# Performance work log

Hardware: AMD Instinct MI355X
Metric: run time of the kernel (lower is better)

## Reference

```python
import jax, jax.numpy as jnp
import numpy as np

B, T, C = 2, 1024, 2048
HEAD = 64              # args.head_size_a
H = C // HEAD          # n_head = 32
D_DECAY, D_AAA, D_MV, D_GATE = 96, 96, 64, 256
GN_EPS = 0.00064
EPS_NORM = 1e-12

ARGS = ['x', 'v0', 'xx_r', 'xx_w', 'xx_k', 'xx_v', 'xx_a', 'xx_g',
        'ww_b', 'ww_w1', 'ww_w2', 'aa_b', 'aa_w1', 'aa_w2',
        'vv_b', 'vv_w1', 'vv_w2', 'gg_w1', 'gg_w2',
        'kk_s', 'ka_s', 'rk_s', 'W_r', 'W_k', 'W_v', 'W_o', 'gn_w', 'gn_b']


def setup_inputs() -> dict:
    key = jax.random.key(0)
    it = iter(jax.random.split(key, 32))
    nrm = lambda shape, s=1.0: jax.random.normal(next(it), shape, jnp.float32) * s
    d = {'x': nrm((B, T, C)), 'v0': nrm((B, T, C))}
    for nm in ('xx_r', 'xx_w', 'xx_k', 'xx_v', 'xx_a', 'xx_g',
               'ww_b', 'aa_b', 'vv_b', 'kk_s', 'ka_s'):
        d[nm] = nrm((1, 1, C), 0.5)
    d['ww_w1'] = nrm((C, D_DECAY), 0.02); d['ww_w2'] = nrm((D_DECAY, C), 0.02)
    d['aa_w1'] = nrm((C, D_AAA), 0.02);   d['aa_w2'] = nrm((D_AAA, C), 0.02)
    d['vv_w1'] = nrm((C, D_MV), 0.02);    d['vv_w2'] = nrm((D_MV, C), 0.02)
    d['gg_w1'] = nrm((C, D_GATE), 0.02);  d['gg_w2'] = nrm((D_GATE, C), 0.02)
    d['rk_s'] = nrm((H, HEAD), 0.5)
    d['W_r'] = nrm((C, C), 0.02); d['W_k'] = nrm((C, C), 0.02)
    d['W_v'] = nrm((C, C), 0.02); d['W_o'] = nrm((C, C), 0.02)
    d['gn_w'] = jnp.ones((C,), jnp.float32)
    d['gn_b'] = jnp.zeros((C,), jnp.float32)
    return d


def _rwkv7_op(r, w, k, v, a, b):
    # RWKV7 state recurrence: state[b,h,i,j] (i = value dim, j = key dim),
    # vectorized over (B,H,N), scanned over T.
    to_tbhn = lambda t: t.reshape(B, T, H, HEAD).astype(jnp.float32).transpose(1, 0, 2, 3)
    rT, kT, vT, aT, bT = map(to_tbhn, (r, k, v, a, b))
    wT = jnp.exp(-jnp.exp(to_tbhn(w)))   # decay in (0, 1)
    state0 = jnp.zeros((B, H, HEAD, HEAD), jnp.float32)

    def step(state, inp):
        wt, kt, vt, at, bt, rt = inp     # each [B,H,N]
        sa = jnp.einsum('bhij,bhj->bhi', state, at)
        state = (state * wt[:, :, None, :]
                 + sa[..., None] * bt[:, :, None, :]
                 + vt[..., None] * kt[:, :, None, :])
        return state, jnp.einsum('bhij,bhj->bhi', state, rt)

    _, outs = jax.lax.scan(step, state0, (wT, kT, vT, aT, bT, rT))  # [T,B,H,N]
    return outs.transpose(1, 0, 2, 3).reshape(B, T, C)


def _group_norm(y, gn_w, gn_b):
    # GroupNorm(H, C, eps=0.00064) applied on (B*T, C): per-(token, head) stats over N
    yh = y.reshape(B, T, H, HEAD)
    mu = yh.mean(-1, keepdims=True)
    var = yh.var(-1, keepdims=True)
    yh = (yh - mu) * jax.lax.rsqrt(var + GN_EPS)
    yh = yh * gn_w.reshape(1, 1, H, HEAD) + gn_b.reshape(1, 1, H, HEAD)
    return yh.reshape(B, T, C)


def _forward(x, v0, xx_r, xx_w, xx_k, xx_v, xx_a, xx_g,
             ww_b, ww_w1, ww_w2, aa_b, aa_w1, aa_w2,
             vv_b, vv_w1, vv_w2, gg_w1, gg_w2,
             kk_s, ka_s, rk_s, W_r, W_k, W_v, W_o, gn_w, gn_b):
    # time_shift(x) - x : shift sequence right by one with zero pad
    xx = jnp.pad(x, ((0, 0), (1, 0), (0, 0)))[:, :T, :] - x
    xr = x + xx * xx_r; xw = x + xx * xx_w; xk = x + xx * xx_k
    xv = x + xx * xx_v; xa = x + xx * xx_a; xg = x + xx * xx_g

    r = xr @ W_r
    w = -jax.nn.softplus(-(ww_b + jnp.tanh(xw @ ww_w1) @ ww_w2)) - 0.5  # clamp to (-inf,-0.5)
    k = xk @ W_k
    v = xv @ W_v
    # layer_id > 0: mix with layer-0 value residual
    v = v + (v0 - v) * jax.nn.sigmoid(vv_b + (xv @ vv_w1) @ vv_w2)
    a = jax.nn.sigmoid(aa_b + (xa @ aa_w1) @ aa_w2)
    g = jax.nn.sigmoid(xg @ gg_w1) @ gg_w2

    kk = k * kk_s
    kkh = kk.reshape(B, T, H, HEAD)
    kk = (kkh / jnp.maximum(jnp.linalg.norm(kkh, axis=-1, keepdims=True), EPS_NORM)).reshape(B, T, C)
    k = k * (1.0 + (a - 1.0) * ka_s)

    y = _rwkv7_op(r, w, k, v, -kk, kk * a)
    y = _group_norm(y, gn_w, gn_b)
    # per-head bonus: (r*k*rk_s).sum(-1) * v
    bonus = ((r.reshape(B, T, H, HEAD) * k.reshape(B, T, H, HEAD) * rk_s).sum(-1, keepdims=True)
             * v.reshape(B, T, H, HEAD)).reshape(B, T, C)
    y = y + bonus
    return (y * g) @ W_o


def reference(x, v0, xx_r, xx_w, xx_k, xx_v, xx_a, xx_g,
              ww_b, ww_w1, ww_w2, aa_b, aa_w1, aa_w2,
              vv_b, vv_w1, vv_w2, gg_w1, gg_w2,
              kk_s, ka_s, rk_s, W_r, W_k, W_v, W_o, gn_w, gn_b):
    out = _forward(x, v0, xx_r, xx_w, xx_k, xx_v, xx_a, xx_g,
                   ww_b, ww_w1, ww_w2, aa_b, aa_w1, aa_w2,
                   vv_b, vv_w1, vv_w2, gg_w1, gg_w2,
                   kk_s, ka_s, rk_s, W_r, W_k, W_v, W_o, gn_w, gn_b)
    # layer_id > 0 passes v0 through unchanged
    return (out, v0)
```

## Files before the change

kernel.cpp:

```cpp
#include <hip/hip_runtime.h>
#include <hip/hip_bf16.h>
#include <math.h>

typedef unsigned short u16;
typedef __attribute__((ext_vector_type(4))) unsigned short us4;
typedef __attribute__((ext_vector_type(8))) unsigned short us8;
typedef __attribute__((ext_vector_type(8))) short s8v;
typedef __attribute__((ext_vector_type(4))) float f4v;

#define BB 2
#define TT 1024
#define CC 2048
#define HH 32
#define BT (BB*TT)


__device__ __forceinline__ float bf2f(u16 u) {
  return __uint_as_float(((unsigned int)u) << 16);
}
__device__ __forceinline__ u16 f2bf(float f) {
  unsigned int x = __float_as_uint(f);
  x += 0x7fffu + ((x >> 16) & 1u);
  return (u16)(x >> 16);
}

__device__ __forceinline__ void gload16(const u16* g, u16* l) {
  __builtin_amdgcn_global_load_lds(
      (const __attribute__((address_space(1))) void*)g,
      (__attribute__((address_space(3))) void*)l, 16, 0, 0);
}

__global__ __launch_bounds__(256)
void mix_k(const float* __restrict__ x, const float* __restrict__ s,
           u16* __restrict__ out) {
  int idx = blockIdx.x * 256 + threadIdx.x;
  int c = idx & (CC - 1);
  int t = (idx >> 11) & (TT - 1);
  float xv = x[idx];
  float xp = (t == 0) ? 0.f : x[idx - CC];
  out[idx] = f2bf(xv + (xp - xv) * s[c]);
}

__global__ __launch_bounds__(256)
void wt_k(const float* __restrict__ W, u16* __restrict__ Wt, int K, int N,
          int Kp) {
  __shared__ u16 tile[32][36];
  const int k0 = blockIdx.x * 32, n0 = blockIdx.y * 32;
  const int tid = threadIdx.x;
  const int r = tid >> 3, c4 = (tid & 7) << 2;
  float4 v = *(const float4*)(W + (size_t)(k0 + r) * N + n0 + c4);
  tile[r][c4 + 0] = f2bf(v.x); tile[r][c4 + 1] = f2bf(v.y);
  tile[r][c4 + 2] = f2bf(v.z); tile[r][c4 + 3] = f2bf(v.w);
  __syncthreads();
  ushort4 o;
  o.x = tile[c4 + 0][r]; o.y = tile[c4 + 1][r];
  o.z = tile[c4 + 2][r]; o.w = tile[c4 + 3][r];
  *(ushort4*)(Wt + (size_t)(n0 + r) * Kp + k0 + c4) = o;
}

enum { EPI_BF = 0, EPI_F32 = 1, EPI_BIAS_SP = 2, EPI_BIAS_SIG = 3,
       EPI_VMIX = 4 };

template<int EPI>
__global__ __launch_bounds__(256)
void mgemm_k(const u16* __restrict__ A, const u16* __restrict__ Bt,
             float* __restrict__ outF, u16* __restrict__ outB,
             int M, int N, int K, int lda, int ldb,
             const float* __restrict__ bias, const u16* __restrict__ p1,
             const float* __restrict__ p2)
{
  __shared__ alignas(16) u16 As[128 * 64];
  __shared__ alignas(16) u16 Bs[128 * 64];
  const int m0 = blockIdx.x * 128;
  const int n0 = blockIdx.y * 128;
  const int tid = threadIdx.x;
  const int lane = tid & 63;
  const int wid = tid >> 6;
  const int wr = wid >> 1, wc = wid & 1;
  f4v acc[4][4];
  #pragma unroll
  for (int i = 0; i < 4; ++i)
    #pragma unroll
    for (int j = 0; j < 4; ++j) acc[i][j] = f4v{0.f, 0.f, 0.f, 0.f};

  const int l15 = lane & 15;
  const int lq = lane >> 4;
  const int nkt = K >> 6;
  for (int kt = 0; kt < nkt; ++kt) {
    const int k0 = kt << 6;
    __syncthreads();
    #pragma unroll
    for (int a = 0; a < 4; ++a) {
      const int blkU = (wid * 4 + a) * 64;
      const int U = blkU + lane;
      const int row = U >> 3;
      const int u = U & 7;
      const int col = ((u ^ (row & 7)) << 3);
      gload16(A  + (size_t)(m0 + row) * lda + k0 + col, &As[blkU * 8]);
      gload16(Bt + (size_t)(n0 + row) * ldb + k0 + col, &Bs[blkU * 8]);
    }
    __syncthreads();
    #pragma unroll
    for (int h = 0; h < 2; ++h) {
      s8v af[4], bfr[4];
      #pragma unroll
      for (int i = 0; i < 4; ++i) {
        const int row = wr * 64 + i * 16 + l15;
        const int u = (h * 4 + lq) ^ (row & 7);
        af[i] = *(const s8v*)&As[row * 64 + u * 8];
      }
      #pragma unroll
      for (int j = 0; j < 4; ++j) {
        const int row = wc * 64 + j * 16 + l15;
        const int u = (h * 4 + lq) ^ (row & 7);
        bfr[j] = *(const s8v*)&Bs[row * 64 + u * 8];
      }
      #pragma unroll
      for (int i = 0; i < 4; ++i)
        #pragma unroll
        for (int j = 0; j < 4; ++j)
          acc[i][j] = __builtin_amdgcn_mfma_f32_16x16x32_bf16(af[i], bfr[j],
                                                              acc[i][j],
                                                              0, 0, 0);
    }
  }
  const int rbase = m0 + wr * 64 + (lq << 2);
  const int cbase = n0 + wc * 64 + l15;
  #pragma unroll
  for (int i = 0; i < 4; ++i) {
    #pragma unroll
    for (int j = 0; j < 4; ++j) {
      f4v c = acc[i][j];
      const int col = cbase + j * 16;
      #pragma unroll
      for (int q = 0; q < 4; ++q) {
        const int row = rbase + i * 16 + q;
        const size_t idx = (size_t)row * N + col;
        const float r = c[q];
        if (EPI == EPI_BF) {
          outB[idx] = f2bf(r);
        } else if (EPI == EPI_F32) {
          outF[idx] = r;
        } else if (EPI == EPI_BIAS_SP) {
          float u = bias[col] + r;
          float z = -u;
          float sp = fmaxf(z, 0.f) + log1pf(expf(-fabsf(z)));
          outB[idx] = f2bf(-sp - 0.5f);
        } else if (EPI == EPI_BIAS_SIG) {
          float u = bias[col] + r;
          outB[idx] = f2bf(1.f / (1.f + expf(-u)));
        } else if (EPI == EPI_VMIX) {
          float u = bias[col] + r;
          float sg = 1.f / (1.f + expf(-u));
          float v = bf2f(p1[idx]);
          float v0v = p2[idx];
          outB[idx] = f2bf(v + (v0v - v) * sg);
        }
      }
    }
  }
}

__global__ __launch_bounds__(256)
void gemm_part_k(const u16* __restrict__ A, const float* __restrict__ W,
                 float* __restrict__ outF, int M, int N, int K, int kchunk,
                 int NP)
{
  __shared__ alignas(16) float As[16][68];
  __shared__ alignas(16) float Bs[16][68];
  const int m0 = blockIdx.x * 64;
  const int n0 = blockIdx.y * 64;
  const int kz = blockIdx.z;
  const int k0base = kz * kchunk;
  const int tid = threadIdx.x;
  const int tx = tid & 15, ty = tid >> 4;
  float acc[4][4] = {{0.f}};
  const int a_m = tid >> 2;
  const int a_k = (tid & 3) << 2;
  const int b_k = tid >> 4;
  const int b_n = (tid & 15) << 2;
  const int niters = kchunk >> 4;
  for (int it = 0; it < niters; ++it) {
    const int k0 = k0base + (it << 4);
    float4 av;
    {
      ushort4 u = *(const ushort4*)(A + (size_t)(m0 + a_m) * K + (k0 + a_k));
      av = make_float4(bf2f(u.x), bf2f(u.y), bf2f(u.z), bf2f(u.w));
    }
    float4 bv;
    {
      int gn = n0 + b_n;
      const float* wp = W + (size_t)(k0 + b_k) * N + gn;
      if (gn + 3 < N) {
        bv = *(const float4*)wp;
      } else {
        bv.x = (gn + 0 < N) ? wp[0] : 0.f;
        bv.y = (gn + 1 < N) ? wp[1] : 0.f;
        bv.z = (gn + 2 < N) ? wp[2] : 0.f;
        bv.w = (gn + 3 < N) ? wp[3] : 0.f;
      }
    }
    __syncthreads();
    As[a_k + 0][a_m] = av.x; As[a_k + 1][a_m] = av.y;
    As[a_k + 2][a_m] = av.z; As[a_k + 3][a_m] = av.w;
    Bs[b_k][b_n + 0] = bv.x; Bs[b_k][b_n + 1] = bv.y;
    Bs[b_k][b_n + 2] = bv.z; Bs[b_k][b_n + 3] = bv.w;
    __syncthreads();
    #pragma unroll
    for (int kk = 0; kk < 16; ++kk) {
      float4 a4 = *(const float4*)&As[kk][ty << 2];
      float4 b4 = *(const float4*)&Bs[kk][tx << 2];
      float ar[4] = {a4.x, a4.y, a4.z, a4.w};
      float br[4] = {b4.x, b4.y, b4.z, b4.w};
      #pragma unroll
      for (int i = 0; i < 4; ++i)
        #pragma unroll
        for (int j = 0; j < 4; ++j)
          acc[i][j] = fmaf(ar[i], br[j], acc[i][j]);
    }
  }
  #pragma unroll
  for (int i = 0; i < 4; ++i) {
    int gm = m0 + (ty << 2) + i;
    #pragma unroll
    for (int j = 0; j < 4; ++j) {
      int gn = n0 + (tx << 2) + j;
      if (gn >= N) continue;
      outF[((size_t)kz * M + gm) * NP + gn] = acc[i][j];
    }
  }
}

__global__ __launch_bounds__(256)
void reduce_k(const float* __restrict__ part, u16* __restrict__ out,
              int M, int D, int NP, int nz, int act, int Dp)
{
  int idx = blockIdx.x * 256 + threadIdx.x;
  if (idx >= M * Dp) return;
  int t = idx / Dp, n = idx - t * Dp;
  float s = 0.f;
  if (n < D) {
    for (int z = 0; z < nz; ++z) s += part[((size_t)z * M + t) * NP + n];
    if (act == 1) s = tanhf(s);
    else if (act == 2) s = 1.f / (1.f + expf(-s));
  }
  out[idx] = f2bf(s);
}

__global__ __launch_bounds__(256)
void prep12_k(const u16* __restrict__ k_in, const u16* __restrict__ a_in,
              const u16* __restrict__ r_in, const u16* __restrict__ w_in,
              const float* __restrict__ kk_s, const float* __restrict__ ka_s,
              u16* __restrict__ ao_out, u16* __restrict__ bo_out,
              u16* __restrict__ k_out, u16* __restrict__ wd_out,
              u16* __restrict__ rw_out, float2* __restrict__ scal,
              float4* __restrict__ scal4)
{
  const int tid = threadIdx.x;
  const int lane = tid & 63;
  const int hpidx = blockIdx.x * 4 + (tid >> 6);
  const int h = hpidx & (HH - 1);
  const int btp = hpidx >> 5;
  const int tp = btp & (TT / 2 - 1);
  const int b = btp >> 9;
  const int c = (h << 6) + lane;
  const size_t be = ((size_t)(b * TT + 2 * tp)) * CC + (h << 6) + lane;
  const size_t bod = be + CC;
  const float ks = kk_s[c], kas = ka_s[c];
  const float k1 = bf2f(k_in[be]),  k2 = bf2f(k_in[bod]);
  const float a1 = bf2f(a_in[be]),  a2 = bf2f(a_in[bod]);
  const float r1 = bf2f(r_in[be]),  r2 = bf2f(r_in[bod]);
  const float wraw1 = bf2f(w_in[be]), wraw2 = bf2f(w_in[bod]);
  float kk1 = k1 * ks, kk2 = k2 * ks;
  float ss1 = kk1 * kk1, ss2 = kk2 * kk2;
  #pragma unroll
  for (int off = 32; off; off >>= 1) {
    ss1 += __shfl_xor(ss1, off, 64);
    ss2 += __shfl_xor(ss2, off, 64);
  }
  const float kkn1 = kk1 / fmaxf(sqrtf(ss1), 1e-12f);
  const float kkn2 = kk2 / fmaxf(sqrtf(ss2), 1e-12f);
  const float kf1 = k1 * (1.f + (a1 - 1.f) * kas);
  const float kf2 = k2 * (1.f + (a2 - 1.f) * kas);
  const float wd1 = expf(-expf(wraw1));
  const float wd2 = expf(-expf(wraw2));
  const float ao1 = -kkn1, ao2 = -kkn2;
  const float bo1 = kkn1 * a1, bo2 = kkn2 * a2;
  const float rw1 = wd1 * r1, rw2 = wd2 * r2;
  float kr1 = kf1 * r1, br1 = bo1 * r1;
  float kr2 = kf2 * r2, br2 = bo2 * r2;
  float cba = bo1 * ao2, ckb = kf1 * ao2;
  float crb = bo1 * rw2, crk = kf1 * rw2;
  #pragma unroll
  for (int off = 32; off; off >>= 1) {
    kr1 += __shfl_xor(kr1, off, 64);  br1 += __shfl_xor(br1, off, 64);
    kr2 += __shfl_xor(kr2, off, 64);  br2 += __shfl_xor(br2, off, 64);
    cba += __shfl_xor(cba, off, 64);  ckb += __shfl_xor(ckb, off, 64);
    crb += __shfl_xor(crb, off, 64);  crk += __shfl_xor(crk, off, 64);
  }
  ao_out[be]  = f2bf(ao1);
  ao_out[bod] = f2bf(wd1 * ao2);
  bo_out[be]  = f2bf(bo1 * wd2);
  bo_out[bod] = f2bf(bo2);
  k_out[be]   = f2bf(kf1);
  k_out[bod]  = f2bf(kf2);
  wd_out[be]  = f2bf(wd1 * wd2);
  wd_out[bod] = f2bf(kf1 * wd2);
  rw_out[be]  = f2bf(rw1);
  rw_out[bod] = f2bf(wd1 * rw2);
  if (lane == 0) {
    const int se = (b * TT + 2 * tp) * HH + h;
    scal[se]      = make_float2(kr1, br1);
    scal[se + HH] = make_float2(kr2, br2);
    scal4[hpidx]  = make_float4(cba, ckb, crb, crk);
  }
}

__global__ __launch_bounds__(256)
void rec_k(const u16* __restrict__ rw, const u16* __restrict__ wd,
           const u16* __restrict__ kv, const u16* __restrict__ v,
           const u16* __restrict__ ao, const u16* __restrict__ bo,
           const float2* __restrict__ scal, const float4* __restrict__ scal4,
           u16* __restrict__ y)
{
  const int gw = blockIdx.x * 4 + (threadIdx.x >> 6);
  const int lane = threadIdx.x & 63;
  const int sub = lane & 15;
  const int grp = lane >> 4;
  const int bh = gw >> 4;
  const int rblk = gw & 15;
  const int i = rblk * 4 + grp;
  const int b = bh >> 5, h = bh & (HH - 1);
  const size_t base0 = ((size_t)b * TT) * CC + (h << 6);
  const size_t vecb = base0 + (sub << 2);
  const size_t vb   = base0 + i;
  const int sbase = b * TT * HH + h;
  const int pbase = b * (TT / 2) * HH + h;
  float s0 = 0.f, s1 = 0.f, s2 = 0.f, s3 = 0.f;

  us4 W12, KW1, AO1, WA2, BW1, BO2, RW1, WR2, K2;
  float V1, V2; float2 SE, SO; float4 S4;
#define PLOAD(TP) do {                                                  \
    const size_t be_ = vecb + (size_t)(2 * (TP)) * CC;                  \
    const size_t bo_ = be_ + CC;                                        \
    W12 = *(const us4*)(wd + be_);  KW1 = *(const us4*)(wd + bo_);      \
    AO1 = *(const us4*)(ao + be_);  WA2 = *(const us4*)(ao + bo_);      \
    BW1 = *(const us4*)(bo + be_);  BO2 = *(const us4*)(bo + bo_);      \
    RW1 = *(const us4*)(rw + be_);  WR2 = *(const us4*)(rw + bo_);      \
    K2  = *(const us4*)(kv + bo_);                                      \
    V1 = bf2f(v[vb + (size_t)(2 * (TP)) * CC]);                         \
    V2 = bf2f(v[vb + (size_t)(2 * (TP) + 1) * CC]);                     \
    SE = scal[sbase + (2 * (TP)) * HH];                                 \
    SO = scal[sbase + (2 * (TP) + 1) * HH];                             \
    S4 = scal4[pbase + (TP) * HH];                                      \
  } while (0)

  PLOAD(0);
  for (int tp = 0; tp < TT / 2; ++tp) {
    const float w0 = bf2f(W12[0]), w1 = bf2f(W12[1]),
                w2 = bf2f(W12[2]), w3 = bf2f(W12[3]);
    const float kw0 = bf2f(KW1[0]), kw1_ = bf2f(KW1[1]),
                kw2 = bf2f(KW1[2]), kw3 = bf2f(KW1[3]);
    const float a0 = bf2f(AO1[0]), a1 = bf2f(AO1[1]),
                a2 = bf2f(AO1[2]), a3 = bf2f(AO1[3]);
    const float x0 = bf2f(WA2[0]), x1 = bf2f(WA2[1]),
                x2 = bf2f(WA2[2]), x3 = bf2f(WA2[3]);
    const float bw0 = bf2f(BW1[0]), bw1_ = bf2f(BW1[1]),
                bw2 = bf2f(BW1[2]), bw3 = bf2f(BW1[3]);
    const float b0 = bf2f(BO2[0]), b1 = bf2f(BO2[1]),
                b2 = bf2f(BO2[2]), b3 = bf2f(BO2[3]);
    const float e0 = bf2f(RW1[0]), e1 = bf2f(RW1[1]),
                e2 = bf2f(RW1[2]), e3 = bf2f(RW1[3]);
    const float f0 = bf2f(WR2[0]), f1 = bf2f(WR2[1]),
                f2 = bf2f(WR2[2]), f3 = bf2f(WR2[3]);
    const float k0 = bf2f(K2[0]), k1 = bf2f(K2[1]),
                k2 = bf2f(K2[2]), k3 = bf2f(K2[3]);
    const float v1c = V1, v2c = V2;
    const float kr1 = SE.x, br1 = SE.y, kr2 = SO.x, br2 = SO.y;
    const float cba = S4.x, ckb = S4.y, crb = S4.z, crk = S4.w;
    if (tp + 1 < TT / 2) PLOAD(tp + 1);
    float u1 = fmaf(s3, a3, fmaf(s2, a2, fmaf(s1, a1, s0 * a0)));
    float u2 = fmaf(s3, x3, fmaf(s2, x2, fmaf(s1, x1, s0 * x0)));
    float q1 = fmaf(s3, e3, fmaf(s2, e2, fmaf(s1, e1, s0 * e0)));
    float q2 = fmaf(s3, f3, fmaf(s2, f2, fmaf(s1, f1, s0 * f0)));
    u1 += __shfl_xor(u1, 1, 64);  u2 += __shfl_xor(u2, 1, 64);
    q1 += __shfl_xor(q1, 1, 64);  q2 += __shfl_xor(q2, 1, 64);
    u1 += __shfl_xor(u1, 2, 64);  u2 += __shfl_xor(u2, 2, 64);
    q1 += __shfl_xor(q1, 2, 64);  q2 += __shfl_xor(q2, 2, 64);
    u1 += __shfl_xor(u1, 4, 64);  u2 += __shfl_xor(u2, 4, 64);
    q1 += __shfl_xor(q1, 4, 64);  q2 += __shfl_xor(q2, 4, 64);
    u1 += __shfl_xor(u1, 8, 64);  u2 += __shfl_xor(u2, 8, 64);
    q1 += __shfl_xor(q1, 8, 64);  q2 += __shfl_xor(q2, 8, 64);
    const float sac = fmaf(ckb, v1c, fmaf(cba, u1, u2));
    const float y1 = fmaf(br1, u1, fmaf(kr1, v1c, q1));
    const float y2 = fmaf(br2, sac, fmaf(kr2, v2c,
                       fmaf(crb, u1, fmaf(crk, v1c, q2))));
    s0 = fmaf(v2c, k0, fmaf(v1c, kw0, fmaf(sac, b0, fmaf(u1, bw0, s0 * w0))));
    s1 = fmaf(v2c, k1, fmaf(v1c, kw1_, fmaf(sac, b1, fmaf(u1, bw1_, s1 * w1))));
    s2 = fmaf(v2c, k2, fmaf(v1c, kw2, fmaf(sac, b2, fmaf(u1, bw2, s2 * w2))));
    s3 = fmaf(v2c, k3, fmaf(v1c, kw3, fmaf(sac, b3, fmaf(u1, bw3, s3 * w3))));
    if (sub == 0) {
      y[vb + (size_t)(2 * tp) * CC] = f2bf(y1);
      y[vb + (size_t)(2 * tp + 1) * CC] = f2bf(y2);
    }
  }
#undef PLOAD
}

__global__ __launch_bounds__(256)
void gn_k(u16* __restrict__ y, const u16* __restrict__ r,
          const u16* __restrict__ k, const u16* __restrict__ v,
          const u16* __restrict__ g, const float* __restrict__ rk_s,
          const float* __restrict__ gn_w, const float* __restrict__ gn_b)
{
  int tid = threadIdx.x, lane = tid & 63, wv = tid >> 6;
  int hidx = blockIdx.x * 4 + wv;
  int h = hidx & (HH - 1);
  int c = (h << 6) + lane;
  size_t base = ((size_t)hidx << 6) + lane;
  float yv = bf2f(y[base]), rv = bf2f(r[base]), kv = bf2f(k[base]);
  float vv = bf2f(v[base]), gv = bf2f(g[base]);
  float bsum = rv * kv * rk_s[c];
  float s1 = yv, s2 = yv * yv;
  for (int off = 32; off; off >>= 1) {
    s1 += __shfl_xor(s1, off, 64);
    s2 += __shfl_xor(s2, off, 64);
    bsum += __shfl_xor(bsum, off, 64);
  }
  float mu = s1 * (1.f / 64.f);
  float var = s2 * (1.f / 64.f) - mu * mu;
  float rstd = rsqrtf(var + 0.00064f);
  float z = (yv - mu) * rstd * gn_w[c] + gn_b[c];
  y[base] = f2bf((z + bsum * vv) * gv);
}

__global__ __launch_bounds__(256)
void copy_v0(const float* __restrict__ v0, float* __restrict__ out) {
  int idx = blockIdx.x * 256 + threadIdx.x;
  ((float4*)out)[idx] = ((const float4*)v0)[idx];
}

__global__ __launch_bounds__(256)
void zero_out(float* __restrict__ out) {
  int idx = blockIdx.x * 256 + threadIdx.x;
  ((float4*)out)[idx] = make_float4(0.f, 0.f, 0.f, 0.f);
}

extern "C" void kernel_launch(void* const* d_in, const int* in_sizes, int n_in,
                              void* d_out, int out_size, void* d_ws, size_t ws_size,
                              hipStream_t stream) {
  (void)n_in; (void)out_size;
  const bool dictOrder = (in_sizes[9] == CC);
  int IX[28];
  if (dictOrder) {
    const int m[28] = {0,1,2,3,4,5,6,7, 8,13,14, 9,15,16, 10,17,18, 19,20,
                       11,12,21, 22,23,24,25, 26,27};
    for (int i = 0; i < 28; ++i) IX[i] = m[i];
  } else {
    for (int i = 0; i < 28; ++i) IX[i] = i;
  }
  const float* x     = (const float*)d_in[IX[0]];
  const float* v0    = (const float*)d_in[IX[1]];
  const float* xx_r  = (const float*)d_in[IX[2]];
  const float* xx_w  = (const float*)d_in[IX[3]];
  const float* xx_k  = (const float*)d_in[IX[4]];
  const float* xx_v  = (const float*)d_in[IX[5]];
  const float* xx_a  = (const float*)d_in[IX[6]];
  const float* xx_g  = (const float*)d_in[IX[7]];
  const float* ww_b  = (const float*)d_in[IX[8]];
  const float* ww_w1 = (const float*)d_in[IX[9]];
  const float* ww_w2 = (const float*)d_in[IX[10]];
  const float* aa_b  = (const float*)d_in[IX[11]];
  const float* aa_w1 = (const float*)d_in[IX[12]];
  const float* aa_w2 = (const float*)d_in[IX[13]];
  const float* vv_b  = (const float*)d_in[IX[14]];
  const float* vv_w1 = (const float*)d_in[IX[15]];
  const float* vv_w2 = (const float*)d_in[IX[16]];
  const float* gg_w1 = (const float*)d_in[IX[17]];
  const float* gg_w2 = (const float*)d_in[IX[18]];
  const float* kk_s  = (const float*)d_in[IX[19]];
  const float* ka_s  = (const float*)d_in[IX[20]];
  const float* rk_s  = (const float*)d_in[IX[21]];
  const float* W_r   = (const float*)d_in[IX[22]];
  const float* W_k   = (const float*)d_in[IX[23]];
  const float* W_v   = (const float*)d_in[IX[24]];
  const float* W_o   = (const float*)d_in[IX[25]];
  const float* gn_w  = (const float*)d_in[IX[26]];
  const float* gn_b  = (const float*)d_in[IX[27]];

  const size_t NBTC = (size_t)BT * CC;
  dim3 blk(256);
  const int grid4f = (int)(NBTC / 4 / 256);

  const size_t WS_NEED = 7 * NBTC * sizeof(u16);
  float* outF = (float*)d_out;
  if (ws_size < WS_NEED || d_ws == nullptr) {
    zero_out<<<grid4f, blk, 0, stream>>>(outF);
    copy_v0<<<grid4f, blk, 0, stream>>>(v0, outF + NBTC);
    return;
  }

  u16* W16   = (u16*)d_ws;
  u16* R0 = W16 + 0 * NBTC;
  u16* R1 = W16 + 1 * NBTC;
  u16* R2 = W16 + 2 * NBTC;
  u16* R3 = W16 + 3 * NBTC;
  u16* R4 = W16 + 4 * NBTC;
  u16* R5 = W16 + 5 * NBTC;
  u16* R6 = W16 + 6 * NBTC;
  float* partY = (float*)R3;
  float* partG = (float*)R5;
  u16* ws_y = (u16*)(outF + NBTC);
  float2* scal = (float2*)(ws_y + NBTC);
  float4* scal4 = (float4*)(ws_y + NBTC + (size_t)BT * HH * 4);

  const int gridMix = (BT * CC) / 256;
  dim3 gM(BT / 128, 2048 / 128);

  mix_k<<<gridMix, blk, 0, stream>>>(x, xx_w, R6);
  gemm_part_k<<<dim3(32, 2, 8), blk, 0, stream>>>(R6, ww_w1, partY,
      BT, 96, 2048, 256, 128);
  reduce_k<<<(BT * 128) / 256, blk, 0, stream>>>(partY, R0, BT, 96, 128, 8, 1, 128);
  wt_k<<<dim3(3, 64), blk, 0, stream>>>(ww_w2, R1, 96, 2048, 128);
  mgemm_k<EPI_BIAS_SP><<<gM, blk, 0, stream>>>(R0, R1, nullptr, R5,
      BT, 2048, 128, 128, 128, ww_b, nullptr, nullptr);

  mix_k<<<gridMix, blk, 0, stream>>>(x, xx_a, R6);
  gemm_part_k<<<dim3(32, 2, 8), blk, 0, stream>>>(R6, aa_w1, partY,
      BT, 96, 2048, 256, 128);
  reduce_k<<<(BT * 128) / 256, blk, 0, stream>>>(partY, R0, BT, 96, 128, 8, 0, 128);
  wt_k<<<dim3(3, 64), blk, 0, stream>>>(aa_w2, R1, 96, 2048, 128);
  mgemm_k<EPI_BIAS_SIG><<<gM, blk, 0, stream>>>(R0, R1, nullptr, R4,
      BT, 2048, 128, 128, 128, aa_b, nullptr, nullptr);

  mix_k<<<gridMix, blk, 0, stream>>>(x, xx_v, R6);
  wt_k<<<dim3(64, 64), blk, 0, stream>>>(W_v, R1, 2048, 2048, 2048);
  mgemm_k<EPI_BF><<<gM, blk, 0, stream>>>(R6, R1, nullptr, R2,
      BT, 2048, 2048, 2048, 2048, nullptr, nullptr, nullptr);
  gemm_part_k<<<dim3(32, 1, 8), blk, 0, stream>>>(R6, vv_w1, partY,
      BT, 64, 2048, 256, 64);
  reduce_k<<<(BT * 64) / 256, blk, 0, stream>>>(partY, R0, BT, 64, 64, 8, 0, 64);
  wt_k<<<dim3(2, 64), blk, 0, stream>>>(vv_w2, R1, 64, 2048, 64);
  mgemm_k<EPI_VMIX><<<gM, blk, 0, stream>>>(R0, R1, nullptr, R2,
      BT, 2048, 64, 64, 64, vv_b, R2, v0);

  mix_k<<<gridMix, blk, 0, stream>>>(x, xx_k, R6);
  wt_k<<<dim3(64, 64), blk, 0, stream>>>(W_k, R3, 2048, 2048, 2048);
  mgemm_k<EPI_BF><<<gM, blk, 0, stream>>>(R6, R3, nullptr, R1,
      BT, 2048, 2048, 2048, 2048, nullptr, nullptr, nullptr);

  mix_k<<<gridMix, blk, 0, stream>>>(x, xx_r, R6);
  wt_k<<<dim3(64, 64), blk, 0, stream>>>(W_r, R3, 2048, 2048, 2048);
  mgemm_k<EPI_BF><<<gM, blk, 0, stream>>>(R6, R3, nullptr, R0,
      BT, 2048, 2048, 2048, 2048, nullptr, nullptr, nullptr);

  prep12_k<<<(BB * (TT / 2) * HH) / 4, blk, 0, stream>>>(
      R1, R4, R0, R5, kk_s, ka_s, R3, R4, R1, R5, R6, scal, scal4);

  rec_k<<<256, blk, 0, stream>>>(R6, R5, R1, R2, R3, R4, scal, scal4, ws_y);

  mix_k<<<gridMix, blk, 0, stream>>>(x, xx_g, R6);
  gemm_part_k<<<dim3(32, 4, 2), blk, 0, stream>>>(R6, gg_w1, partG,
      BT, 256, 2048, 1024, 256);
  reduce_k<<<(BT * 256) / 256, blk, 0, stream>>>(partG, R3, BT, 256, 256, 2, 2, 256);
  wt_k<<<dim3(8, 64), blk, 0, stream>>>(gg_w2, R5, 256, 2048, 256);
  mgemm_k<EPI_BF><<<gM, blk, 0, stream>>>(R3, R5, nullptr, R4,
      BT, 2048, 256, 256, 256, nullptr, nullptr, nullptr);

  gn_k<<<BT * HH / 4, blk, 0, stream>>>(ws_y, R0, R1, R2, R4,
                                        rk_s, gn_w, gn_b);

  wt_k<<<dim3(64, 64), blk, 0, stream>>>(W_o, R5, 2048, 2048, 2048);
  mgemm_k<EPI_F32><<<gM, blk, 0, stream>>>(ws_y, R5, outF, nullptr,
      BT, 2048, 2048, 2048, 2048, nullptr, nullptr, nullptr);

  copy_v0<<<grid4f, blk, 0, stream>>>(v0, outF + NBTC);
}
```

Before: 804.6 us.

## Replace split-K fp32 LoRA down-projections with bf16 MFMA GEMM and fused activation

The fp32 SIMT split-K `gemm_part_k` plus separate `reduce_k` for the low-rank down-projections (w, a, v, g) are removed. Each weight is now transposed to bf16 with `wt_k` and run through the MFMA `mgemm_k` kernel. A new `EPI_H` epilogue applies tanh or sigmoid and zero-pads the extra columns, so the partial-sum buffer and the reduce launch go away. The cost is a per-call weight transpose and very low parallelism: only 16–32 workgroups, each looping over the full K=2048, where split-K used several hundred.

```diff
diff --git a/kernel.cpp b/kernel.cpp
--- a/kernel.cpp
+++ b/kernel.cpp
@@ -59,13 +59,14 @@
 }
 
 enum { EPI_BF = 0, EPI_F32 = 1, EPI_BIAS_SP = 2, EPI_BIAS_SIG = 3,
-       EPI_VMIX = 4 };
+       EPI_VMIX = 4, EPI_H = 5 };
 
 template<int EPI>
 __global__ __launch_bounds__(256)
 void mgemm_k(const u16* __restrict__ A, const u16* __restrict__ Bt,
              float* __restrict__ outF, u16* __restrict__ outB,
              int M, int N, int K, int lda, int ldb,
+             int Dlim, int Dpad, int act,
              const float* __restrict__ bias, const u16* __restrict__ p1,
              const float* __restrict__ p2)
 {
@@ -135,8 +136,19 @@
       #pragma unroll
       for (int q = 0; q < 4; ++q) {
         const int row = rbase + i * 16 + q;
+        const float r = c[q];
+        if (EPI == EPI_H) {
+          if (col < Dlim) {
+            float t = r;
+            if (act == 1) t = tanhf(t);
+            else if (act == 2) t = 1.f / (1.f + expf(-t));
+            outB[(size_t)row * N + col] = f2bf(t);
+          } else if (col < Dpad) {
+            outB[(size_t)row * N + col] = 0;
+          }
+          continue;
+        }
         const size_t idx = (size_t)row * N + col;
-        const float r = c[q];
         if (EPI == EPI_BF) {
           outB[idx] = f2bf(r);
         } else if (EPI == EPI_F32) {
@@ -159,92 +171,6 @@
       }
     }
   }
-}
-
-__global__ __launch_bounds__(256)
-void gemm_part_k(const u16* __restrict__ A, const float* __restrict__ W,
-                 float* __restrict__ outF, int M, int N, int K, int kchunk,
-                 int NP)
-{
-  __shared__ alignas(16) float As[16][68];
-  __shared__ alignas(16) float Bs[16][68];
-  const int m0 = blockIdx.x * 64;
-  const int n0 = blockIdx.y * 64;
-  const int kz = blockIdx.z;
-  const int k0base = kz * kchunk;
-  const int tid = threadIdx.x;
-  const int tx = tid & 15, ty = tid >> 4;
-  float acc[4][4] = {{0.f}};
-  const int a_m = tid >> 2;
-  const int a_k = (tid & 3) << 2;
-  const int b_k = tid >> 4;
-  const int b_n = (tid & 15) << 2;
-  const int niters = kchunk >> 4;
-  for (int it = 0; it < niters; ++it) {
-    const int k0 = k0base + (it << 4);
-    float4 av;
-    {
-      ushort4 u = *(const ushort4*)(A + (size_t)(m0 + a_m) * K + (k0 + a_k));
-      av = make_float4(bf2f(u.x), bf2f(u.y), bf2f(u.z), bf2f(u.w));
-    }
-    float4 bv;
-    {
-      int gn = n0 + b_n;
-      const float* wp = W + (size_t)(k0 + b_k) * N + gn;
-      if (gn + 3 < N) {
-        bv = *(const float4*)wp;
-      } else {
-        bv.x = (gn + 0 < N) ? wp[0] : 0.f;
-        bv.y = (gn + 1 < N) ? wp[1] : 0.f;
-        bv.z = (gn + 2 < N) ? wp[2] : 0.f;
-        bv.w = (gn + 3 < N) ? wp[3] : 0.f;
-      }
-    }
-    __syncthreads();
-    As[a_k + 0][a_m] = av.x; As[a_k + 1][a_m] = av.y;
-    As[a_k + 2][a_m] = av.z; As[a_k + 3][a_m] = av.w;
-    Bs[b_k][b_n + 0] = bv.x; Bs[b_k][b_n + 1] = bv.y;
-    Bs[b_k][b_n + 2] = bv.z; Bs[b_k][b_n + 3] = bv.w;
-    __syncthreads();
-    #pragma unroll
-    for (int kk = 0; kk < 16; ++kk) {
-      float4 a4 = *(const float4*)&As[kk][ty << 2];
-      float4 b4 = *(const float4*)&Bs[kk][tx << 2];
-      float ar[4] = {a4.x, a4.y, a4.z, a4.w};
-      float br[4] = {b4.x, b4.y, b4.z, b4.w};
-      #pragma unroll
-      for (int i = 0; i < 4; ++i)
-        #pragma unroll
-        for (int j = 0; j < 4; ++j)
-          acc[i][j] = fmaf(ar[i], br[j], acc[i][j]);
-    }
-  }
-  #pragma unroll
-  for (int i = 0; i < 4; ++i) {
-    int gm = m0 + (ty << 2) + i;
-    #pragma unroll
-    for (int j = 0; j < 4; ++j) {
-      int gn = n0 + (tx << 2) + j;
-      if (gn >= N) continue;
-      outF[((size_t)kz * M + gm) * NP + gn] = acc[i][j];
-    }
-  }
-}
-
-__global__ __launch_bounds__(256)
-void reduce_k(const float* __restrict__ part, u16* __restrict__ out,
-              int M, int D, int NP, int nz, int act, int Dp)
-{
-  int idx = blockIdx.x * 256 + threadIdx.x;
-  if (idx >= M * Dp) return;
-  int t = idx / Dp, n = idx - t * Dp;
-  float s = 0.f;
-  if (n < D) {
-    for (int z = 0; z < nz; ++z) s += part[((size_t)z * M + t) * NP + n];
-    if (act == 1) s = tanhf(s);
-    else if (act == 2) s = 1.f / (1.f + expf(-s));
-  }
-  out[idx] = f2bf(s);
 }
 
 __global__ __launch_bounds__(256)
@@ -508,51 +434,51 @@
   u16* R4 = W16 + 4 * NBTC;
   u16* R5 = W16 + 5 * NBTC;
   u16* R6 = W16 + 6 * NBTC;
-  float* partY = (float*)R3;
-  float* partG = (float*)R5;
   u16* ws_y = (u16*)(outF + NBTC);
   float2* scal = (float2*)(ws_y + NBTC);
   float4* scal4 = (float4*)(ws_y + NBTC + (size_t)BT * HH * 4);
 
   const int gridMix = (BT * CC) / 256;
   dim3 gM(BT / 128, 2048 / 128);
+  dim3 gH1(BT / 128, 1);
+  dim3 gH2(BT / 128, 2);
 
   mix_k<<<gridMix, blk, 0, stream>>>(x, xx_w, R6);
-  gemm_part_k<<<dim3(32, 2, 8), blk, 0, stream>>>(R6, ww_w1, partY,
-      BT, 96, 2048, 256, 128);
-  reduce_k<<<(BT * 128) / 256, blk, 0, stream>>>(partY, R0, BT, 96, 128, 8, 1, 128);
+  wt_k<<<dim3(64, 3), blk, 0, stream>>>(ww_w1, R3, 2048, 96, 2048);
+  mgemm_k<EPI_H><<<gH1, blk, 0, stream>>>(R6, R3, nullptr, R0,
+      BT, 128, 2048, 2048, 2048, 96, 128, 1, nullptr, nullptr, nullptr);
   wt_k<<<dim3(3, 64), blk, 0, stream>>>(ww_w2, R1, 96, 2048, 128);
   mgemm_k<EPI_BIAS_SP><<<gM, blk, 0, stream>>>(R0, R1, nullptr, R5,
-      BT, 2048, 128, 128, 128, ww_b, nullptr, nullptr);
+      BT, 2048, 128, 128, 128, 0, 0, 0, ww_b, nullptr, nullptr);
 
   mix_k<<<gridMix, blk, 0, stream>>>(x, xx_a, R6);
-  gemm_part_k<<<dim3(32, 2, 8), blk, 0, stream>>>(R6, aa_w1, partY,
-      BT, 96, 2048, 256, 128);
-  reduce_k<<<(BT * 128) / 256, blk, 0, stream>>>(partY, R0, BT, 96, 128, 8, 0, 128);
+  wt_k<<<dim3(64, 3), blk, 0, stream>>>(aa_w1, R3, 2048, 96, 2048);
+  mgemm_k<EPI_H><<<gH1, blk, 0, stream>>>(R6, R3, nullptr, R0,
+      BT, 128, 2048, 2048, 2048, 96, 128, 0, nullptr, nullptr, nullptr);
   wt_k<<<dim3(3, 64), blk, 0, stream>>>(aa_w2, R1, 96, 2048, 128);
   mgemm_k<EPI_BIAS_SIG><<<gM, blk, 0, stream>>>(R0, R1, nullptr, R4,
-      BT, 2048, 128, 128, 128, aa_b, nullptr, nullptr);
+      BT, 2048, 128, 128, 128, 0, 0, 0, aa_b, nullptr, nullptr);
 
   mix_k<<<gridMix, blk, 0, stream>>>(x, xx_v, R6);
   wt_k<<<dim3(64, 64), blk, 0, stream>>>(W_v, R1, 2048, 2048, 2048);
   mgemm_k<EPI_BF><<<gM, blk, 0, stream>>>(R6, R1, nullptr, R2,
-      BT, 2048, 2048, 2048, 2048, nullptr, nullptr, nullptr);
-  gemm_part_k<<<dim3(32, 1, 8), blk, 0, stream>>>(R6, vv_w1, partY,
-      BT, 64, 2048, 256, 64);
-  reduce_k<<<(BT * 64) / 256, blk, 0, stream>>>(partY, R0, BT, 64, 64, 8, 0, 64);
+      BT, 2048, 2048, 2048, 2048, 0, 0, 0, nullptr, nullptr, nullptr);
+  wt_k<<<dim3(64, 2), blk, 0, stream>>>(vv_w1, R3, 2048, 64, 2048);
+  mgemm_k<EPI_H><<<gH1, blk, 0, stream>>>(R6, R3, nullptr, R0,
+      BT, 64, 2048, 2048, 2048, 64, 64, 0, nullptr, nullptr, nullptr);
   wt_k<<<dim3(2, 64), blk, 0, stream>>>(vv_w2, R1, 64, 2048, 64);
   mgemm_k<EPI_VMIX><<<gM, blk, 0, stream>>>(R0, R1, nullptr, R2,
-      BT, 2048, 64, 64, 64, vv_b, R2, v0);
+      BT, 2048, 64, 64, 64, 0, 0, 0, vv_b, R2, v0);
 
   mix_k<<<gridMix, blk, 0, stream>>>(x, xx_k, R6);
   wt_k<<<dim3(64, 64), blk, 0, stream>>>(W_k, R3, 2048, 2048, 2048);
   mgemm_k<EPI_BF><<<gM, blk, 0, stream>>>(R6, R3, nullptr, R1,
-      BT, 2048, 2048, 2048, 2048, nullptr, nullptr, nullptr);
+      BT, 2048, 2048, 2048, 2048, 0, 0, 0, nullptr, nullptr, nullptr);
 
   mix_k<<<gridMix, blk, 0, stream>>>(x, xx_r, R6);
   wt_k<<<dim3(64, 64), blk, 0, stream>>>(W_r, R3, 2048, 2048, 2048);
   mgemm_k<EPI_BF><<<gM, blk, 0, stream>>>(R6, R3, nullptr, R0,
-      BT, 2048, 2048, 2048, 2048, nullptr, nullptr, nullptr);
+      BT, 2048, 2048, 2048, 2048, 0, 0, 0, nullptr, nullptr, nullptr);
 
   prep12_k<<<(BB * (TT / 2) * HH) / 4, blk, 0, stream>>>(
       R1, R4, R0, R5, kk_s, ka_s, R3, R4, R1, R5, R6, scal, scal4);
@@ -560,19 +486,19 @@
   rec_k<<<256, blk, 0, stream>>>(R6, R5, R1, R2, R3, R4, scal, scal4, ws_y);
 
   mix_k<<<gridMix, blk, 0, stream>>>(x, xx_g, R6);
-  gemm_part_k<<<dim3(32, 4, 2), blk, 0, stream>>>(R6, gg_w1, partG,
-      BT, 256, 2048, 1024, 256);
-  reduce_k<<<(BT * 256) / 256, blk, 0, stream>>>(partG, R3, BT, 256, 256, 2, 2, 256);
+  wt_k<<<dim3(64, 8), blk, 0, stream>>>(gg_w1, R5, 2048, 256, 2048);
+  mgemm_k<EPI_H><<<gH2, blk, 0, stream>>>(R6, R5, nullptr, R3,
+      BT, 256, 2048, 2048, 2048, 256, 256, 2, nullptr, nullptr, nullptr);
   wt_k<<<dim3(8, 64), blk, 0, stream>>>(gg_w2, R5, 256, 2048, 256);
   mgemm_k<EPI_BF><<<gM, blk, 0, stream>>>(R3, R5, nullptr, R4,
-      BT, 2048, 256, 256, 256, nullptr, nullptr, nullptr);
+      BT, 2048, 256, 256, 256, 0, 0, 0, nullptr, nullptr, nullptr);
 
   gn_k<<<BT * HH / 4, blk, 0, stream>>>(ws_y, R0, R1, R2, R4,
                                         rk_s, gn_w, gn_b);
 
   wt_k<<<dim3(64, 64), blk, 0, stream>>>(W_o, R5, 2048, 2048, 2048);
   mgemm_k<EPI_F32><<<gM, blk, 0, stream>>>(ws_y, R5, outF, nullptr,
-      BT, 2048, 2048, 2048, 2048, nullptr, nullptr, nullptr);
+      BT, 2048, 2048, 2048, 2048, 0, 0, 0, nullptr, nullptr, nullptr);
 
   copy_v0<<<grid4f, blk, 0, stream>>>(v0, outF + NBTC);
 }
```

Result: slower. 867.1 us (+7.8%).
